# Optimization experiments

Hardware: AMD Instinct MI355X
Metric: run time of the kernel (lower is better)

The kernel has to match this reference:

```python
import jax, jax.numpy as jnp
import numpy as np

DIM_H = 1024
DIM_S = 1024
DIM_U = 1024
DIM_Z = 128
DT_OVER_TAU = 0.1  # dt=0.1, tau=1
GAIN = 4.0


def setup_inputs() -> dict:
    key = jax.random.key(0)
    k = jax.random.split(key, 5)
    B, T = 128, 512
    h0 = jax.random.normal(k[0], (B, DIM_H), dtype=jnp.float32)
    s_seq = jax.random.normal(k[1], (B, T, DIM_S), dtype=jnp.float32)
    u_seq = jax.random.normal(k[2], (B, T, DIM_U), dtype=jnp.float32)
    # parameters per torch init
    W = jax.random.normal(k[3], (DIM_H, DIM_H), dtype=jnp.float32) * (GAIN / np.sqrt(DIM_H))
    b = jnp.zeros((DIM_H,), dtype=jnp.float32)
    Bs = jnp.eye(DIM_H, DIM_S, dtype=jnp.float32)
    Bu = jnp.eye(DIM_H, DIM_U, dtype=jnp.float32)
    Wz = jax.random.normal(k[4], (DIM_Z, DIM_H), dtype=jnp.float32) * (1.0 / np.sqrt(DIM_Z))
    bz = jnp.zeros((DIM_Z,), dtype=jnp.float32)
    return {"h0": h0, "s_seq": s_seq, "u_seq": u_seq, "W": W, "b": b,
            "Bs": Bs, "Bu": Bu, "Wz": Wz, "bz": bz}


def reference(h0, s_seq, u_seq, W, b, Bs, Bu, Wz, bz):
    a = DT_OVER_TAU
    # Precompute input drive for all timesteps: Bs@s_t + Bu@u_t + b  -> [B,T,H]
    drive = jnp.einsum('hs,bts->bth', Bs, s_seq) + jnp.einsum('hu,btu->bth', Bu, u_seq) + b
    # Only steps t=0..T-2 are consumed to produce h_1..h_{T-1}
    drive_t = jnp.swapaxes(drive[:, :-1, :], 0, 1)  # [T-1,B,H]

    def step(h, d):
        h_next = (1.0 - a) * h + a * jnp.tanh(h @ W.T + d)
        return h_next, h_next

    _, hs = jax.lax.scan(step, h0, drive_t)          # hs: [T-1,B,H]
    h_seq = jnp.concatenate([h0[:, None, :], jnp.swapaxes(hs, 0, 1)], axis=1)  # [B,T,H]
    z_seq = jnp.einsum('zh,bth->btz', Wz, h_seq) + bz                          # [B,T,Z]
    return h_seq, z_seq
```

## Files before the change

kernel.cpp:

```cpp
#include <hip/hip_runtime.h>
#include <cstdint>
#include <cmath>

#define DIM_H 1024
#define DIM_Z 128
#define NBATCH 128
#define NT 512
#define A_DT   0.1f
#define OMA_DT 0.9f

typedef short bf16x8 __attribute__((ext_vector_type(8)));
typedef float f32x4  __attribute__((ext_vector_type(4)));
#define MFMA16 __builtin_amdgcn_mfma_f32_16x16x32_bf16

#define HX_BYTE_OFF 16384
#define HX_PAR_U32  131072

__device__ __forceinline__ void store_u32_dev(unsigned* p, unsigned v){
  asm volatile("global_store_dword %0, %1, off sc0 sc1" :: "v"(p), "v"(v) : "memory");
}
__device__ __forceinline__ uint4 load_u4_dev(const unsigned* p){
  uint4 r;
  asm volatile("global_load_dwordx4 %0, %1, off sc0 sc1" : "=v"(r) : "v"(p) : "memory");
  return r;
}
__device__ __forceinline__ unsigned load_u32_dev(const unsigned* p){
  unsigned r;
  asm volatile("global_load_dword %0, %1, off sc0 sc1\n\ts_waitcnt vmcnt(0)"
               : "=v"(r) : "v"(p) : "memory");
  return r;
}
__device__ __forceinline__ void wait_vm0(){
  asm volatile("s_waitcnt vmcnt(0)" ::: "memory");
}
__device__ __forceinline__ unsigned cvt_pk_bf16(float a, float b){
  unsigned r;
  asm("v_cvt_pk_bf16_f32 %0, %1, %2" : "=v"(r) : "v"(a), "v"(b));
  return r;
}
__device__ __forceinline__ unsigned pack_hl(float h){
  unsigned t = cvt_pk_bf16(h, h);
  float res = h - __uint_as_float(t << 16);
  return cvt_pk_bf16(h, res);
}

__global__ void k_init(unsigned* w){
  int i = blockIdx.x*1024 + threadIdx.x;
  store_u32_dev(w + i, (i == 0) ? 1u : 0u);
}

__global__ void k_check(const float* __restrict__ Bs, const float* __restrict__ Bu,
                        const float* __restrict__ bias, unsigned* w){
  const size_t n1 = (size_t)DIM_H * DIM_H;
  const size_t total = 2*n1 + DIM_H;
  bool bad = false;
  for (size_t e = (size_t)blockIdx.x*blockDim.x + threadIdx.x; e < total;
       e += (size_t)gridDim.x*blockDim.x){
    float v, ex;
    if (e < n1)       { v = Bs[e];      ex = ((e>>10)==(e&1023)) ? 1.f : 0.f; }
    else if (e < 2*n1){ size_t e2=e-n1; v = Bu[e2]; ex = ((e2>>10)==(e2&1023)) ? 1.f : 0.f; }
    else              { v = bias[e-2*n1]; ex = 0.f; }
    if (v != ex) bad = true;
  }
  if (bad) atomicAnd(&w[0], 0u);
}

__global__ void k_drive_general(const float* __restrict__ s_seq, const float* __restrict__ u_seq,
                                const float* __restrict__ Bs, const float* __restrict__ Bu,
                                const float* __restrict__ bias, float* __restrict__ hseq,
                                const unsigned* __restrict__ w){
  if (w[0]) return;
  __shared__ float sl[DIM_H], ul[DIM_H];
  for (int pt = blockIdx.x; pt < NBATCH*(NT-1); pt += gridDim.x){
    int b = pt/(NT-1), t = pt%(NT-1);
    const float* sp = s_seq + ((size_t)b*NT + t)*DIM_H;
    const float* up = u_seq + ((size_t)b*NT + t)*DIM_H;
    __syncthreads();
    for (int k = threadIdx.x; k < DIM_H; k += blockDim.x){ sl[k]=sp[k]; ul[k]=up[k]; }
    __syncthreads();
    for (int r = threadIdx.x; r < DIM_H; r += blockDim.x){
      float acc = bias[r];
      const float* br = Bs + (size_t)r*DIM_H;
      const float* cr = Bu + (size_t)r*DIM_H;
      for (int k=0;k<DIM_H;k++) acc = fmaf(br[k], sl[k], acc);
      for (int k=0;k<DIM_H;k++) acc = fmaf(cr[k], ul[k], acc);
      hseq[((size_t)b*NT + (t+1))*DIM_H + r] = acc;
    }
  }
}

__attribute__((amdgpu_flat_work_group_size(256,256)))
__attribute__((amdgpu_waves_per_eu(1)))
__global__ void k_rnn(const float* __restrict__ h0, const float* __restrict__ s_seq,
                      const float* __restrict__ u_seq, const float* __restrict__ W,
                      const float* __restrict__ bias, float* __restrict__ hseq,
                      unsigned* __restrict__ wsp){
  const int tid  = threadIdx.x;
  const int lane = tid & 63;
  const int kq   = tid >> 6;
  const int g    = blockIdx.x >> 5;
  const int rb   = blockIdx.x & 31;
  const int row0 = rb * 32;
  const int b0   = g * 16;
  unsigned* prog = wsp + 64 + g*128;
  const int fast = (int)wsp[0];
  unsigned* hx32 = (unsigned*)((char*)wsp + HX_BYTE_OFF);

  __shared__ __align__(16) unsigned WL[2][2][32][256];
  __shared__ __align__(16) float LP[2][2][4][64][4];

  {
    const int crl = tid >> 3;
    const int rt = crl >> 4, lr = crl & 15;
    const int kbase = (tid & 7) * 128;
    const float* wr = W + (size_t)(row0 + crl)*DIM_H + kbase;
    for (int kk = 0; kk < 128; kk += 8){
      int k = kbase + kk;
      float4 x = *(const float4*)(wr + kk);
      float4 y = *(const float4*)(wr + kk + 4);
      unsigned h01 = cvt_pk_bf16(x.x, x.y), h23 = cvt_pk_bf16(x.z, x.w);
      unsigned h45 = cvt_pk_bf16(y.x, y.y), h67 = cvt_pk_bf16(y.z, y.w);
      float l0 = x.x - __uint_as_float(h01 << 16);
      float l1 = x.y - __uint_as_float(h01 & 0xffff0000u);
      float l2 = x.z - __uint_as_float(h23 << 16);
      float l3 = x.w - __uint_as_float(h23 & 0xffff0000u);
      float l4 = y.x - __uint_as_float(h45 << 16);
      float l5 = y.y - __uint_as_float(h45 & 0xffff0000u);
      float l6 = y.z - __uint_as_float(h67 << 16);
      float l7 = y.w - __uint_as_float(h67 & 0xffff0000u);
      unsigned L01 = cvt_pk_bf16(l0, l1), L23 = cvt_pk_bf16(l2, l3);
      unsigned L45 = cvt_pk_bf16(l4, l5), L67 = cvt_pk_bf16(l6, l7);
      int c = k >> 5, kg = (k & 31) >> 3, li = kg*16 + lr;
      *(uint4*)&WL[rt][0][c][li*4] = make_uint4(h01, h23, h45, h67);
      *(uint4*)&WL[rt][1][c][li*4] = make_uint4(L01, L23, L45, L67);
    }
  }

  const int rowin = tid & 15;
  const int bl    = tid >> 4;
  const int bb    = b0 + bl;
  const int r0g   = row0 + rowin;
  const int r1g   = row0 + 16 + rowin;
  const int laneC = ((rowin >> 2) << 4) | bl;
  const int regC  = rowin & 3;
  const float bias0 = bias[r0g], bias1 = bias[r1g];

  const size_t loffu = (size_t)(b0 + (lane & 15))*1024 + kq*256 + (lane >> 4)*8;
  const unsigned* pB0 = hx32 + loffu;
  const unsigned* pB1 = hx32 + HX_PAR_U32 + loffu;

  float hold0 = h0[(size_t)bb*DIM_H + r0g];
  float hold1 = h0[(size_t)bb*DIM_H + r1g];
  hseq[((size_t)bb*NT + 0)*DIM_H + r0g] = hold0;
  hseq[((size_t)bb*NT + 0)*DIM_H + r1g] = hold1;
  store_u32_dev(hx32 + (size_t)bb*1024 + r0g, pack_hl(hold0));
  store_u32_dev(hx32 + (size_t)bb*1024 + r1g, pack_hl(hold1));
  float sv0=0.f, uv0=0.f, sv1=0.f, uv1=0.f;
  if (fast){
    size_t o0 = ((size_t)bb*NT + 0)*DIM_H + r0g;
    size_t o1 = ((size_t)bb*NT + 0)*DIM_H + r1g;
    sv0 = s_seq[o0]; uv0 = u_seq[o0];
    sv1 = s_seq[o1]; uv1 = u_seq[o1];
  }
  wait_vm0();
  __syncthreads();
  if (lane == 0) store_u32_dev(prog + rb*4 + kq, 1u);

  for (int t = 0; t < NT-1; t++){
    float dv0, dv1;
    if (fast){
      dv0 = sv0 + uv0 + bias0;
      dv1 = sv1 + uv1 + bias1;
      size_t o0 = ((size_t)bb*NT + (t+1))*DIM_H + r0g;
      size_t o1 = ((size_t)bb*NT + (t+1))*DIM_H + r1g;
      sv0 = s_seq[o0]; uv0 = u_seq[o0];
      sv1 = s_seq[o1]; uv1 = u_seq[o1];
    } else {
      dv0 = hseq[((size_t)bb*NT + (t+1))*DIM_H + r0g];
      dv1 = hseq[((size_t)bb*NT + (t+1))*DIM_H + r1g];
    }

    {
      const unsigned tgt = (unsigned)(t+1);
      const unsigned* pp = prog + kq*32 + lane;
      unsigned v = tgt;
      for(;;){
        if (lane < 32) v = load_u32_dev(pp);
        if (__all(v >= tgt)) break;
        __builtin_amdgcn_s_sleep(1);
      }
    }

    const unsigned* pB = (t & 1) ? pB1 : pB0;
    uint4 sB[8][2];
    #pragma unroll
    for (int ks = 0; ks < 8; ks++){
      sB[ks][0] = load_u4_dev(pB + ks*32);
      sB[ks][1] = load_u4_dev(pB + ks*32 + 4);
    }

    wait_vm0();
    __builtin_amdgcn_sched_barrier(0);

    f32x4 c00{0,0,0,0}, c01{0,0,0,0}, c02{0,0,0,0}, c03{0,0,0,0};
    f32x4 c10{0,0,0,0}, c11{0,0,0,0}, c12{0,0,0,0}, c13{0,0,0,0};
    #pragma unroll
    for (int ks = 0; ks < 8; ks++){
      uint4 wa = sB[ks][0], wb = sB[ks][1];
      uint4 bhu, blu;
      bhu.x = __builtin_amdgcn_perm(wa.y, wa.x, 0x05040100u);
      bhu.y = __builtin_amdgcn_perm(wa.w, wa.z, 0x05040100u);
      bhu.z = __builtin_amdgcn_perm(wb.y, wb.x, 0x05040100u);
      bhu.w = __builtin_amdgcn_perm(wb.w, wb.z, 0x05040100u);
      blu.x = __builtin_amdgcn_perm(wa.y, wa.x, 0x07060302u);
      blu.y = __builtin_amdgcn_perm(wa.w, wa.z, 0x07060302u);
      blu.z = __builtin_amdgcn_perm(wb.y, wb.x, 0x07060302u);
      blu.w = __builtin_amdgcn_perm(wb.w, wb.z, 0x07060302u);
      bf16x8 bh  = __builtin_bit_cast(bf16x8, bhu);
      bf16x8 bl2 = __builtin_bit_cast(bf16x8, blu);
      const int c = kq*8 + ks;
      bf16x8 a0h = *(const bf16x8*)&WL[0][0][c][lane*4];
      bf16x8 a0l = *(const bf16x8*)&WL[0][1][c][lane*4];
      bf16x8 a1h = *(const bf16x8*)&WL[1][0][c][lane*4];
      bf16x8 a1l = *(const bf16x8*)&WL[1][1][c][lane*4];
      c00 = MFMA16(a0h, bh,  c00, 0,0,0);
      c01 = MFMA16(a0h, bl2, c01, 0,0,0);
      c02 = MFMA16(a0l, bh,  c02, 0,0,0);
      c03 = MFMA16(a0l, bl2, c03, 0,0,0);
      c10 = MFMA16(a1h, bh,  c10, 0,0,0);
      c11 = MFMA16(a1h, bl2, c11, 0,0,0);
      c12 = MFMA16(a1l, bh,  c12, 0,0,0);
      c13 = MFMA16(a1l, bl2, c13, 0,0,0);
    }
    f32x4 C0 = (c00 + c01) + (c02 + c03);
    f32x4 C1 = (c10 + c11) + (c12 + c13);
    const int lpp = t & 1;
    *(f32x4*)&LP[lpp][0][kq][lane][0] = C0;
    *(f32x4*)&LP[lpp][1][kq][lane][0] = C1;
    __syncthreads();

    float pre0 = (LP[lpp][0][0][laneC][regC] + LP[lpp][0][1][laneC][regC])
               + (LP[lpp][0][2][laneC][regC] + LP[lpp][0][3][laneC][regC]);
    float pre1 = (LP[lpp][1][0][laneC][regC] + LP[lpp][1][1][laneC][regC])
               + (LP[lpp][1][2][laneC][regC] + LP[lpp][1][3][laneC][regC]);
    float hn0 = OMA_DT*hold0 + A_DT*tanhf(pre0 + dv0);
    float hn1 = OMA_DT*hold1 + A_DT*tanhf(pre1 + dv1);
    hold0 = hn0; hold1 = hn1;
    {
      unsigned* hq = hx32 + (((t+1) & 1) ? HX_PAR_U32 : 0) + (size_t)bb*1024;
      store_u32_dev(hq + r0g, pack_hl(hn0));
      store_u32_dev(hq + r1g, pack_hl(hn1));
    }
    wait_vm0();
    if (lane == 0) store_u32_dev(prog + rb*4 + kq, (unsigned)(t+2));
    hseq[((size_t)bb*NT + (t+1))*DIM_H + r0g] = hn0;
    hseq[((size_t)bb*NT + (t+1))*DIM_H + r1g] = hn1;
  }
}

#define GLD_LDS16(gp, lp) \
  __builtin_amdgcn_global_load_lds((const __attribute__((address_space(1))) void*)(gp), \
                                   (__attribute__((address_space(3))) void*)(lp), 16, 0, 0)
#define DOT4(hv, wv, a) do { \
  a = fmaf((hv).x, (wv).x, a); a = fmaf((hv).y, (wv).y, a); \
  a = fmaf((hv).z, (wv).z, a); a = fmaf((hv).w, (wv).w, a); } while(0)

__device__ __forceinline__ float wave_sum64(float x){
  x += __int_as_float(__builtin_amdgcn_update_dpp(0, __float_as_int(x), 0x111, 0xf, 0xf, true));
  x += __int_as_float(__builtin_amdgcn_update_dpp(0, __float_as_int(x), 0x112, 0xf, 0xf, true));
  x += __int_as_float(__builtin_amdgcn_update_dpp(0, __float_as_int(x), 0x114, 0xf, 0xf, true));
  x += __int_as_float(__builtin_amdgcn_update_dpp(0, __float_as_int(x), 0x118, 0xf, 0xf, true));
  x += __int_as_float(__builtin_amdgcn_update_dpp(0, __float_as_int(x), 0x142, 0xf, 0xf, true));
  x += __int_as_float(__builtin_amdgcn_update_dpp(0, __float_as_int(x), 0x143, 0xf, 0xf, true));
  return x;
}

__launch_bounds__(256, 1)
__global__ void k_z(const float* __restrict__ hseq, const float* __restrict__ Wz,
                    const float* __restrict__ bz, float* __restrict__ z){
  const int tid = threadIdx.x, lane = tid & 63, wv = tid >> 6;
  const size_t pos0 = (size_t)blockIdx.x * 16;
  __shared__ __align__(16) float h_lds[16*DIM_H];
  __shared__ __align__(16) float out_lds[512];
  #pragma unroll
  for (int i=0;i<16;i++){
    const float* src = hseq + (pos0+i)*DIM_H + tid*4;
    GLD_LDS16(src, &h_lds[i*DIM_H + tid*4]);
  }
  asm volatile("s_waitcnt vmcnt(0)" ::: "memory");
  __syncthreads();
  const int ei = tid>>5, er = tid&31;
  for (int zg=0; zg<4; zg++){
    const int zr0 = zg*32;
    float4 wreg[8][4];
    const float* wr = Wz + (size_t)(zr0 + wv*8)*DIM_H + lane*4;
    #pragma unroll
    for (int rr=0;rr<8;rr++)
      #pragma unroll
      for (int c=0;c<4;c++)
        wreg[rr][c] = *(const float4*)(wr + (size_t)rr*DIM_H + c*256);
    #pragma unroll 2
    for (int i=0;i<16;i++){
      const float4* hp = (const float4*)&h_lds[i*DIM_H];
      float4 hv0 = hp[lane], hv1 = hp[lane+64], hv2 = hp[lane+128], hv3 = hp[lane+192];
      float acc[8];
      #pragma unroll
      for (int rr=0;rr<8;rr++){
        float s = 0.f;
        DOT4(hv0, wreg[rr][0], s); DOT4(hv1, wreg[rr][1], s);
        DOT4(hv2, wreg[rr][2], s); DOT4(hv3, wreg[rr][3], s);
        acc[rr] = s;
      }
      #pragma unroll
      for (int rr=0;rr<8;rr++){
        float v = wave_sum64(acc[rr]);
        if (lane==63) out_lds[wv*128 + i*8 + rr] = v;
      }
    }
    __syncthreads();
    const int zr = zr0 + er;
    float v1 = out_lds[(er>>3)*128 + ei*8     + (er&7)] + bz[zr];
    float v2 = out_lds[(er>>3)*128 + (ei+8)*8 + (er&7)] + bz[zr];
    z[(pos0+ei)*DIM_Z + zr]   = v1;
    z[(pos0+ei+8)*DIM_Z + zr] = v2;
    __syncthreads();
  }
}

extern "C" void kernel_launch(void* const* d_in, const int* in_sizes, int n_in,
                              void* d_out, int out_size, void* d_ws, size_t ws_size,
                              hipStream_t stream){
  const float* h0    = (const float*)d_in[0];
  const float* s_seq = (const float*)d_in[1];
  const float* u_seq = (const float*)d_in[2];
  const float* W     = (const float*)d_in[3];
  const float* bias  = (const float*)d_in[4];
  const float* Bs    = (const float*)d_in[5];
  const float* Bu    = (const float*)d_in[6];
  const float* Wz    = (const float*)d_in[7];
  const float* bz    = (const float*)d_in[8];
  float* hseq = (float*)d_out;
  float* z    = hseq + (size_t)NBATCH*NT*DIM_H;
  unsigned* w = (unsigned*)d_ws;

  k_init<<<4, 1024, 0, stream>>>(w);
  k_check<<<256, 256, 0, stream>>>(Bs, Bu, bias, w);
  k_drive_general<<<2048, 256, 0, stream>>>(s_seq, u_seq, Bs, Bu, bias, hseq, w);
  {
    void* args[] = {(void*)&h0, (void*)&s_seq, (void*)&u_seq, (void*)&W,
                    (void*)&bias, (void*)&hseq, (void*)&w};
    hipError_t rc = hipLaunchCooperativeKernel((const void*)k_rnn, dim3(256), dim3(256),
                                               args, 0, stream);
    if (rc != hipSuccess){
      k_rnn<<<256, 256, 0, stream>>>(h0, s_seq, u_seq, W, bias, hseq, w);
    }
  }
  k_z<<<(NBATCH*NT)/16, 256, 0, stream>>>(hseq, Wz, bz, z);
}
```

Baseline: 2.868 ms.

## Pair adjacent hidden rows per thread and relax cache scope on hx exchange

```diff
diff --git a/kernel.cpp b/kernel.cpp
--- a/kernel.cpp
+++ b/kernel.cpp
@@ -19,15 +19,19 @@
 __device__ __forceinline__ void store_u32_dev(unsigned* p, unsigned v){
   asm volatile("global_store_dword %0, %1, off sc0 sc1" :: "v"(p), "v"(v) : "memory");
 }
-__device__ __forceinline__ uint4 load_u4_dev(const unsigned* p){
-  uint4 r;
-  asm volatile("global_load_dwordx4 %0, %1, off sc0 sc1" : "=v"(r) : "v"(p) : "memory");
-  return r;
-}
 __device__ __forceinline__ unsigned load_u32_dev(const unsigned* p){
   unsigned r;
   asm volatile("global_load_dword %0, %1, off sc0 sc1\n\ts_waitcnt vmcnt(0)"
                : "=v"(r) : "v"(p) : "memory");
+  return r;
+}
+__device__ __forceinline__ void store2_hx(unsigned* p, unsigned a, unsigned b){
+  unsigned long long v = ((unsigned long long)b << 32) | a;
+  asm volatile("global_store_dwordx2 %0, %1, off sc1" :: "v"(p), "v"(v) : "memory");
+}
+__device__ __forceinline__ uint4 load_u4_hx(const unsigned* p){
+  uint4 r;
+  asm volatile("global_load_dwordx4 %0, %1, off sc1" : "=v"(r) : "v"(p) : "memory");
   return r;
 }
 __device__ __forceinline__ void wait_vm0(){
@@ -136,31 +140,31 @@
     }
   }
 
-  const int rowin = tid & 15;
-  const int bl    = tid >> 4;
-  const int bb    = b0 + bl;
-  const int r0g   = row0 + rowin;
-  const int r1g   = row0 + 16 + rowin;
-  const int laneC = ((rowin >> 2) << 4) | bl;
-  const int regC  = rowin & 3;
-  const float bias0 = bias[r0g], bias1 = bias[r1g];
+  const int rwp = tid & 15;
+  const int bl  = tid >> 4;
+  const int bb  = b0 + bl;
+  const int R0  = 2*rwp;
+  const int tle = rwp >> 3;
+  const int r0in = R0 & 15;
+  const int laneC = ((r0in >> 2) << 4) | bl;
+  const int regC  = r0in & 3;
+  const int rg0 = row0 + R0;
+  const float bias0 = bias[rg0], bias1 = bias[rg0 + 1];
 
   const size_t loffu = (size_t)(b0 + (lane & 15))*1024 + kq*256 + (lane >> 4)*8;
   const unsigned* pB0 = hx32 + loffu;
   const unsigned* pB1 = hx32 + HX_PAR_U32 + loffu;
 
-  float hold0 = h0[(size_t)bb*DIM_H + r0g];
-  float hold1 = h0[(size_t)bb*DIM_H + r1g];
-  hseq[((size_t)bb*NT + 0)*DIM_H + r0g] = hold0;
-  hseq[((size_t)bb*NT + 0)*DIM_H + r1g] = hold1;
-  store_u32_dev(hx32 + (size_t)bb*1024 + r0g, pack_hl(hold0));
-  store_u32_dev(hx32 + (size_t)bb*1024 + r1g, pack_hl(hold1));
+  float hold0 = h0[(size_t)bb*DIM_H + rg0];
+  float hold1 = h0[(size_t)bb*DIM_H + rg0 + 1];
+  *(float2*)&hseq[((size_t)bb*NT + 0)*DIM_H + rg0] = make_float2(hold0, hold1);
+  store2_hx(hx32 + (size_t)bb*1024 + rg0, pack_hl(hold0), pack_hl(hold1));
   float sv0=0.f, uv0=0.f, sv1=0.f, uv1=0.f;
   if (fast){
-    size_t o0 = ((size_t)bb*NT + 0)*DIM_H + r0g;
-    size_t o1 = ((size_t)bb*NT + 0)*DIM_H + r1g;
-    sv0 = s_seq[o0]; uv0 = u_seq[o0];
-    sv1 = s_seq[o1]; uv1 = u_seq[o1];
+    size_t o = ((size_t)bb*NT + 0)*DIM_H + rg0;
+    float2 s2 = *(const float2*)(s_seq + o);
+    float2 u2 = *(const float2*)(u_seq + o);
+    sv0 = s2.x; sv1 = s2.y; uv0 = u2.x; uv1 = u2.y;
   }
   wait_vm0();
   __syncthreads();
@@ -171,13 +175,13 @@
     if (fast){
       dv0 = sv0 + uv0 + bias0;
       dv1 = sv1 + uv1 + bias1;
-      size_t o0 = ((size_t)bb*NT + (t+1))*DIM_H + r0g;
-      size_t o1 = ((size_t)bb*NT + (t+1))*DIM_H + r1g;
-      sv0 = s_seq[o0]; uv0 = u_seq[o0];
-      sv1 = s_seq[o1]; uv1 = u_seq[o1];
+      size_t o = ((size_t)bb*NT + (t+1))*DIM_H + rg0;
+      float2 s2 = *(const float2*)(s_seq + o);
+      float2 u2 = *(const float2*)(u_seq + o);
+      sv0 = s2.x; sv1 = s2.y; uv0 = u2.x; uv1 = u2.y;
     } else {
-      dv0 = hseq[((size_t)bb*NT + (t+1))*DIM_H + r0g];
-      dv1 = hseq[((size_t)bb*NT + (t+1))*DIM_H + r1g];
+      float2 d2 = *(const float2*)(hseq + ((size_t)bb*NT + (t+1))*DIM_H + rg0);
+      dv0 = d2.x; dv1 = d2.y;
     }
 
     {
@@ -195,8 +199,8 @@
     uint4 sB[8][2];
     #pragma unroll
     for (int ks = 0; ks < 8; ks++){
-      sB[ks][0] = load_u4_dev(pB + ks*32);
-      sB[ks][1] = load_u4_dev(pB + ks*32 + 4);
+      sB[ks][0] = load_u4_hx(pB + ks*32);
+      sB[ks][1] = load_u4_hx(pB + ks*32 + 4);
     }
 
     wait_vm0();
@@ -239,22 +243,20 @@
     *(f32x4*)&LP[lpp][1][kq][lane][0] = C1;
     __syncthreads();
 
-    float pre0 = (LP[lpp][0][0][laneC][regC] + LP[lpp][0][1][laneC][regC])
-               + (LP[lpp][0][2][laneC][regC] + LP[lpp][0][3][laneC][regC]);
-    float pre1 = (LP[lpp][1][0][laneC][regC] + LP[lpp][1][1][laneC][regC])
-               + (LP[lpp][1][2][laneC][regC] + LP[lpp][1][3][laneC][regC]);
+    float pre0 = (LP[lpp][tle][0][laneC][regC]   + LP[lpp][tle][1][laneC][regC])
+               + (LP[lpp][tle][2][laneC][regC]   + LP[lpp][tle][3][laneC][regC]);
+    float pre1 = (LP[lpp][tle][0][laneC][regC+1] + LP[lpp][tle][1][laneC][regC+1])
+               + (LP[lpp][tle][2][laneC][regC+1] + LP[lpp][tle][3][laneC][regC+1]);
     float hn0 = OMA_DT*hold0 + A_DT*tanhf(pre0 + dv0);
     float hn1 = OMA_DT*hold1 + A_DT*tanhf(pre1 + dv1);
     hold0 = hn0; hold1 = hn1;
     {
-      unsigned* hq = hx32 + (((t+1) & 1) ? HX_PAR_U32 : 0) + (size_t)bb*1024;
-      store_u32_dev(hq + r0g, pack_hl(hn0));
-      store_u32_dev(hq + r1g, pack_hl(hn1));
+      unsigned* hq = hx32 + (((t+1) & 1) ? HX_PAR_U32 : 0) + (size_t)bb*1024 + rg0;
+      store2_hx(hq, pack_hl(hn0), pack_hl(hn1));
     }
     wait_vm0();
     if (lane == 0) store_u32_dev(prog + rb*4 + kq, (unsigned)(t+2));
-    hseq[((size_t)bb*NT + (t+1))*DIM_H + r0g] = hn0;
-    hseq[((size_t)bb*NT + (t+1))*DIM_H + r1g] = hn1;
+    *(float2*)&hseq[((size_t)bb*NT + (t+1))*DIM_H + rg0] = make_float2(hn0, hn1);
   }
 }
 
```

New measurement: 2.987 ms. 1.04x slower.
